# Performance work log

Measured on AMD Instinct MI355X. Metric: run time of the kernel, lower is better.

The kernel has to match this reference:

```python
import jax, jax.numpy as jnp
import numpy as np

N_NODES = 50000
N_EDGES = 800000
IN_FEATS = 64


def setup_inputs() -> dict:
    key = jax.random.key(0)
    k_h, k_src, k_dst, k_w = jax.random.split(key, 4)
    h = jax.random.normal(k_h, (N_NODES, IN_FEATS), dtype=jnp.float32)
    src = jax.random.randint(k_src, (N_EDGES,), 0, N_NODES, dtype=jnp.int64)
    dst = jax.random.randint(k_dst, (N_EDGES,), 0, N_NODES, dtype=jnp.int64)
    W = jax.random.normal(k_w, (1, 2 * IN_FEATS), dtype=jnp.float32) * (1.0 / np.sqrt(2 * IN_FEATS))
    b = jnp.zeros((1,), dtype=jnp.float32)
    return {"h": h, "src": src, "dst": dst, "W": W, "b": b}


def reference(h, src, dst, W, b):
    # Gather per-edge src/dst node features: [E, F] each
    h_u = h[src]
    h_v = h[dst]
    # Linear(cat([h_u, h_v], 1)) == h_u @ W_u^T + h_v @ W_v^T + b
    # (avoids materializing the [E, 2F] concat)
    F_ = h.shape[1]
    W_u = W[:, :F_]   # [1, F]
    W_v = W[:, F_:]   # [1, F]
    logits = jnp.einsum('ef,of->eo', h_u, W_u) + jnp.einsum('ef,of->eo', h_v, W_v) + b  # [E, 1]
    return jax.nn.sigmoid(logits)
```

## Files before the change

kernel.cpp:

```cpp
#include <hip/hip_runtime.h>
#include <math.h>

#define NF 64

__global__ void node_scores_kernel(const float4* __restrict__ h4,
                                   const float4* __restrict__ W4,
                                   float2* __restrict__ S, int nNodes,
                                   const void* __restrict__ src,
                                   int* __restrict__ flag) {
    if (blockIdx.x == 0 && threadIdx.x < 64) {
        const int* p = (const int*)src;
        int v = p[2 * threadIdx.x + 1];
        unsigned long long bal = __ballot(v == 0);
        if (threadIdx.x == 0) *flag = (bal == ~0ull) ? 1 : 0;
    }

    int gtid  = blockIdx.x * blockDim.x + threadIdx.x;
    int wave  = gtid >> 6;
    int lane  = gtid & 63;
    int group = lane >> 4;
    int fl    = lane & 15;
    int node  = wave * 4 + group;
    if (node >= nNodes) return;

    float4 x  = h4[node * 16 + fl];
    float4 wu = W4[fl];
    float4 wv = W4[16 + fl];
    float su = x.x * wu.x + x.y * wu.y + x.z * wu.z + x.w * wu.w;
    float sv = x.x * wv.x + x.y * wv.y + x.z * wv.z + x.w * wv.w;

    #pragma unroll
    for (int off = 1; off < 16; off <<= 1) {
        su += __shfl_xor(su, off, 64);
        sv += __shfl_xor(sv, off, 64);
    }
    if (fl == 0) S[node] = make_float2(su, sv);
}

__global__ void edge_kernel(const void* __restrict__ srcv,
                            const void* __restrict__ dstv,
                            const float2* __restrict__ S,
                            const float* __restrict__ b,
                            const int* __restrict__ flag,
                            float4* __restrict__ out4, int nE4) {
    int t = blockIdx.x * blockDim.x + threadIdx.x;
    if (t >= nE4) return;

    int s0, s1, s2, s3, d0, d1, d2, d3;
    if (*flag) {
        const int4* sp = (const int4*)srcv;
        const int4* dp = (const int4*)dstv;
        int4 a = sp[2 * t], c = sp[2 * t + 1];
        int4 e = dp[2 * t], f = dp[2 * t + 1];
        s0 = a.x; s1 = a.z; s2 = c.x; s3 = c.z;
        d0 = e.x; d1 = e.z; d2 = f.x; d3 = f.z;
    } else {
        int4 a = ((const int4*)srcv)[t];
        int4 e = ((const int4*)dstv)[t];
        s0 = a.x; s1 = a.y; s2 = a.z; s3 = a.w;
        d0 = e.x; d1 = e.y; d2 = e.z; d3 = e.w;
    }

    float2 su0 = S[s0], su1 = S[s1], su2 = S[s2], su3 = S[s3];
    float2 dv0 = S[d0], dv1 = S[d1], dv2 = S[d2], dv3 = S[d3];
    float bias = b[0];

    float l0 = su0.x + dv0.y + bias;
    float l1 = su1.x + dv1.y + bias;
    float l2 = su2.x + dv2.y + bias;
    float l3 = su3.x + dv3.y + bias;

    out4[t] = make_float4(1.0f / (1.0f + __expf(-l0)),
                          1.0f / (1.0f + __expf(-l1)),
                          1.0f / (1.0f + __expf(-l2)),
                          1.0f / (1.0f + __expf(-l3)));
}

extern "C" void kernel_launch(void* const* d_in, const int* in_sizes, int n_in,
                              void* d_out, int out_size, void* d_ws, size_t ws_size,
                              hipStream_t stream) {
    const float* h   = (const float*)d_in[0];
    const void*  src = d_in[1];
    const void*  dst = d_in[2];
    const float* W   = (const float*)d_in[3];
    const float* b   = (const float*)d_in[4];
    float* out = (float*)d_out;

    int nNodes = in_sizes[0] / NF;
    int nE     = in_sizes[1];

    int*    flag = (int*)d_ws;
    float2* S    = (float2*)((char*)d_ws + 256);

    int nodeBlocks = (nNodes + 15) / 16;
    node_scores_kernel<<<nodeBlocks, 256, 0, stream>>>(
        (const float4*)h, (const float4*)W, S, nNodes, src, flag);

    int nE4 = nE / 4;
    int edgeBlocks = (nE4 + 255) / 256;
    edge_kernel<<<edgeBlocks, 256, 0, stream>>>(src, dst, S, b, flag,
                                                (float4*)out, nE4);
}
```

Before: 19.15 us.

## Fuse node-score and edge kernels into one cooperative kernel with grid sync

Merges the per-node score pass and the per-edge gather/sigmoid pass into a single cooperative launch with 1024 persistent blocks that use grid-stride loops and a grid-wide barrier between the phases. Each wave now detects the index width itself instead of reading a flag that one block writes. The aim is to remove the second kernel launch and the gap between the two kernels. In exchange it adds the cost of a cooperative launch and a grid.sync, and the fixed block count limits parallelism in each phase.

```diff
diff --git a/kernel.cpp b/kernel.cpp
--- a/kernel.cpp
+++ b/kernel.cpp
@@ -1,103 +1,98 @@
 #include <hip/hip_runtime.h>
+#include <hip/hip_cooperative_groups.h>
 #include <math.h>
 
+namespace cg = cooperative_groups;
+
 #define NF 64
+#define NBLOCKS 1024
+#define NTHREADS 256
 
-__global__ void node_scores_kernel(const float4* __restrict__ h4,
-                                   const float4* __restrict__ W4,
-                                   float2* __restrict__ S, int nNodes,
-                                   const void* __restrict__ src,
-                                   int* __restrict__ flag) {
-    if (blockIdx.x == 0 && threadIdx.x < 64) {
-        const int* p = (const int*)src;
-        int v = p[2 * threadIdx.x + 1];
-        unsigned long long bal = __ballot(v == 0);
-        if (threadIdx.x == 0) *flag = (bal == ~0ull) ? 1 : 0;
+__global__ void fused_kernel(const float4* __restrict__ h4,
+                             const float4* __restrict__ W4,
+                             float2* __restrict__ S, int nNodes,
+                             const void* __restrict__ srcv,
+                             const void* __restrict__ dstv,
+                             const float* __restrict__ b,
+                             float4* __restrict__ out4, int nE4) {
+    cg::grid_group grid = cg::this_grid();
+
+    int lane = threadIdx.x & 63;
+
+    int odd = ((const int*)srcv)[2 * lane + 1];
+    unsigned long long bal = __ballot(odd == 0);
+    bool is64 = (bal == ~0ull);
+
+    int gtid     = blockIdx.x * blockDim.x + threadIdx.x;
+    int nThreads = gridDim.x * blockDim.x;
+
+    int group = lane >> 4;
+    int fl    = lane & 15;
+    float4 wu = W4[fl];
+    float4 wv = W4[16 + fl];
+    int waveId = gtid >> 6;
+    int nWaves = nThreads >> 6;
+    for (int node = waveId * 4 + group; node < nNodes; node += nWaves * 4) {
+        float4 x = h4[node * 16 + fl];
+        float su = x.x * wu.x + x.y * wu.y + x.z * wu.z + x.w * wu.w;
+        float sv = x.x * wv.x + x.y * wv.y + x.z * wv.z + x.w * wv.w;
+        #pragma unroll
+        for (int off = 1; off < 16; off <<= 1) {
+            su += __shfl_xor(su, off, 64);
+            sv += __shfl_xor(sv, off, 64);
+        }
+        if (fl == 0) S[node] = make_float2(su, sv);
     }
 
-    int gtid  = blockIdx.x * blockDim.x + threadIdx.x;
-    int wave  = gtid >> 6;
-    int lane  = gtid & 63;
-    int group = lane >> 4;
-    int fl    = lane & 15;
-    int node  = wave * 4 + group;
-    if (node >= nNodes) return;
+    grid.sync();
 
-    float4 x  = h4[node * 16 + fl];
-    float4 wu = W4[fl];
-    float4 wv = W4[16 + fl];
-    float su = x.x * wu.x + x.y * wu.y + x.z * wu.z + x.w * wu.w;
-    float sv = x.x * wv.x + x.y * wv.y + x.z * wv.z + x.w * wv.w;
-
-    #pragma unroll
-    for (int off = 1; off < 16; off <<= 1) {
-        su += __shfl_xor(su, off, 64);
-        sv += __shfl_xor(sv, off, 64);
+    float bias = b[0];
+    for (int t = gtid; t < nE4; t += nThreads) {
+        int s0, s1, s2, s3, d0, d1, d2, d3;
+        if (is64) {
+            const int4* sp = (const int4*)srcv;
+            const int4* dp = (const int4*)dstv;
+            int4 a = sp[2 * t], c = sp[2 * t + 1];
+            int4 e = dp[2 * t], f = dp[2 * t + 1];
+            s0 = a.x; s1 = a.z; s2 = c.x; s3 = c.z;
+            d0 = e.x; d1 = e.z; d2 = f.x; d3 = f.z;
+        } else {
+            int4 a = ((const int4*)srcv)[t];
+            int4 e = ((const int4*)dstv)[t];
+            s0 = a.x; s1 = a.y; s2 = a.z; s3 = a.w;
+            d0 = e.x; d1 = e.y; d2 = e.z; d3 = e.w;
+        }
+        float2 A = S[s0], B = S[s1], C = S[s2], D = S[s3];
+        float2 E = S[d0], F = S[d1], G = S[d2], H = S[d3];
+        float l0 = A.x + E.y + bias;
+        float l1 = B.x + F.y + bias;
+        float l2 = C.x + G.y + bias;
+        float l3 = D.x + H.y + bias;
+        out4[t] = make_float4(1.0f / (1.0f + __expf(-l0)),
+                              1.0f / (1.0f + __expf(-l1)),
+                              1.0f / (1.0f + __expf(-l2)),
+                              1.0f / (1.0f + __expf(-l3)));
     }
-    if (fl == 0) S[node] = make_float2(su, sv);
-}
-
-__global__ void edge_kernel(const void* __restrict__ srcv,
-                            const void* __restrict__ dstv,
-                            const float2* __restrict__ S,
-                            const float* __restrict__ b,
-                            const int* __restrict__ flag,
-                            float4* __restrict__ out4, int nE4) {
-    int t = blockIdx.x * blockDim.x + threadIdx.x;
-    if (t >= nE4) return;
-
-    int s0, s1, s2, s3, d0, d1, d2, d3;
-    if (*flag) {
-        const int4* sp = (const int4*)srcv;
-        const int4* dp = (const int4*)dstv;
-        int4 a = sp[2 * t], c = sp[2 * t + 1];
-        int4 e = dp[2 * t], f = dp[2 * t + 1];
-        s0 = a.x; s1 = a.z; s2 = c.x; s3 = c.z;
-        d0 = e.x; d1 = e.z; d2 = f.x; d3 = f.z;
-    } else {
-        int4 a = ((const int4*)srcv)[t];
-        int4 e = ((const int4*)dstv)[t];
-        s0 = a.x; s1 = a.y; s2 = a.z; s3 = a.w;
-        d0 = e.x; d1 = e.y; d2 = e.z; d3 = e.w;
-    }
-
-    float2 su0 = S[s0], su1 = S[s1], su2 = S[s2], su3 = S[s3];
-    float2 dv0 = S[d0], dv1 = S[d1], dv2 = S[d2], dv3 = S[d3];
-    float bias = b[0];
-
-    float l0 = su0.x + dv0.y + bias;
-    float l1 = su1.x + dv1.y + bias;
-    float l2 = su2.x + dv2.y + bias;
-    float l3 = su3.x + dv3.y + bias;
-
-    out4[t] = make_float4(1.0f / (1.0f + __expf(-l0)),
-                          1.0f / (1.0f + __expf(-l1)),
-                          1.0f / (1.0f + __expf(-l2)),
-                          1.0f / (1.0f + __expf(-l3)));
 }
 
 extern "C" void kernel_launch(void* const* d_in, const int* in_sizes, int n_in,
                               void* d_out, int out_size, void* d_ws, size_t ws_size,
                               hipStream_t stream) {
-    const float* h   = (const float*)d_in[0];
-    const void*  src = d_in[1];
-    const void*  dst = d_in[2];
-    const float* W   = (const float*)d_in[3];
-    const float* b   = (const float*)d_in[4];
-    float* out = (float*)d_out;
+    const float4* h4  = (const float4*)d_in[0];
+    const void*   src = d_in[1];
+    const void*   dst = d_in[2];
+    const float4* W4  = (const float4*)d_in[3];
+    const float*  b   = (const float*)d_in[4];
+    float4* out4 = (float4*)d_out;
 
     int nNodes = in_sizes[0] / NF;
-    int nE     = in_sizes[1];
+    int nE4    = in_sizes[1] / 4;
 
-    int*    flag = (int*)d_ws;
-    float2* S    = (float2*)((char*)d_ws + 256);
+    float2* S = (float2*)d_ws;
 
-    int nodeBlocks = (nNodes + 15) / 16;
-    node_scores_kernel<<<nodeBlocks, 256, 0, stream>>>(
-        (const float4*)h, (const float4*)W, S, nNodes, src, flag);
-
-    int nE4 = nE / 4;
-    int edgeBlocks = (nE4 + 255) / 256;
-    edge_kernel<<<edgeBlocks, 256, 0, stream>>>(src, dst, S, b, flag,
-                                                (float4*)out, nE4);
+    void* args[] = { (void*)&h4, (void*)&W4, (void*)&S, (void*)&nNodes,
+                     (void*)&src, (void*)&dst, (void*)&b,
+                     (void*)&out4, (void*)&nE4 };
+    hipLaunchCooperativeKernel((void*)fused_kernel, dim3(NBLOCKS), dim3(NTHREADS),
+                               args, 0, stream);
 }
```

After: 71.36 us. 273% more time.
